# Performance work log

Measured on AMD Instinct MI355X. Metric: run time of the kernel, lower is better.

Reference implementation:

```python
import jax, jax.numpy as jnp
import numpy as np

N_NODES = 50000
N_EDGES = 800000
NUM_GRAPHS = 1024
IN_DIM = 25
DIM = 64
STEPS = 3


def setup_inputs() -> dict:
    key = jax.random.key(0)
    ks = jax.random.split(key, 16)
    s = 0.1
    return {
        "x": jax.random.normal(ks[0], (N_NODES, IN_DIM), dtype=jnp.float32),
        "edge_index": jax.random.randint(ks[1], (2, N_EDGES), 0, N_NODES),
        "batch": jnp.sort(jax.random.randint(ks[2], (N_NODES,), 0, NUM_GRAPHS)),
        "W0": jax.random.normal(ks[3], (IN_DIM, DIM), dtype=jnp.float32) * s,
        "b0": jnp.zeros((DIM,), jnp.float32),
        "Wc": jax.random.normal(ks[4], (DIM, DIM), dtype=jnp.float32) * s,
        "bc": jnp.zeros((DIM,), jnp.float32),
        "Wih": jax.random.normal(ks[5], (4 * DIM, 2 * DIM), dtype=jnp.float32) * s,
        "Whh": jax.random.normal(ks[6], (4 * DIM, DIM), dtype=jnp.float32) * s,
        "bih": jnp.zeros((4 * DIM,), jnp.float32),
        "bhh": jnp.zeros((4 * DIM,), jnp.float32),
        "W1": jax.random.normal(ks[7], (2 * DIM, DIM), dtype=jnp.float32) * s,
        "b1": jnp.zeros((DIM,), jnp.float32),
        "W2": jax.random.normal(ks[8], (DIM, 1), dtype=jnp.float32) * s,
        "b2": jnp.zeros((1,), jnp.float32),
    }


def _lstm_cell(xin, h, c, Wih, Whh, bih, bhh):
    gates = xin @ Wih.T + h @ Whh.T + bih + bhh  # [B, 4*DIM]
    i, f, g, o = jnp.split(gates, 4, axis=-1)
    i, f, o = jax.nn.sigmoid(i), jax.nn.sigmoid(f), jax.nn.sigmoid(o)
    g = jnp.tanh(g)
    c = f * c + i * g
    h = o * jnp.tanh(c)
    return h, c


def reference(x, edge_index, batch, W0, b0, Wc, bc, Wih, Whh, bih, bhh, W1, b1, W2, b2):
    n = x.shape[0]
    # lin0 + relu
    h = jax.nn.relu(x @ W0 + b0)
    # GCNConv: x @ W, add self loops, symmetric normalization, scatter-add
    hw = h @ Wc
    loops = jnp.arange(n, dtype=edge_index.dtype)
    row = jnp.concatenate([edge_index[0], loops])  # sources
    col = jnp.concatenate([edge_index[1], loops])  # targets
    deg = jax.ops.segment_sum(jnp.ones_like(row, dtype=hw.dtype), col, num_segments=n)
    dinv = jnp.where(deg > 0, jax.lax.rsqrt(deg), 0.0)
    norm = dinv[row] * dinv[col]
    msg = hw[row] * norm[:, None]  # [E+N, DIM] gather
    agg = jax.ops.segment_sum(msg, col, num_segments=n) + bc
    h = jax.nn.relu(agg)
    # Set2Set pooling with LSTM, 3 processing steps
    B = NUM_GRAPHS
    q_star = jnp.zeros((B, 2 * DIM), h.dtype)
    hs = jnp.zeros((B, DIM), h.dtype)
    cs = jnp.zeros((B, DIM), h.dtype)
    for _ in range(STEPS):
        hs, cs = _lstm_cell(q_star, hs, cs, Wih, Whh, bih, bhh)
        q = hs  # [B, DIM]
        e = jnp.sum(h * q[batch], axis=-1)  # [N]
        emax = jax.ops.segment_max(e, batch, num_segments=B)
        a = jnp.exp(e - emax[batch])
        asum = jax.ops.segment_sum(a, batch, num_segments=B)
        a = a / asum[batch]
        r = jax.ops.segment_sum(a[:, None] * h, batch, num_segments=B)  # [B, DIM]
        q_star = jnp.concatenate([q, r], axis=-1)
    out = jax.nn.relu(q_star @ W1 + b1)
    out = out @ W2 + b2
    return out.reshape(-1)
```

## Files before the change

### kernel.cpp

```cpp
#include <hip/hip_runtime.h>
#include <hip/hip_fp16.h>
#include <math.h>

#define N_NODES 50000
#define N_EDGES 800000
#define NGRAPH  1024
#define IN_DIM  25
#define DIM     64

#define NBK 98
#define CAP 12288
#define NPB 128
#define NFILL (NBK * 4)
#define NBIN 391
#define CROWS 128

__device__ inline float wsum(float v) {
#pragma unroll
  for (int off = 32; off > 0; off >>= 1) v += __shfl_xor(v, off, 64);
  return v;
}
__device__ inline int wsumi(int v) {
#pragma unroll
  for (int off = 32; off > 0; off >>= 1) v += __shfl_xor(v, off, 64);
  return v;
}
__device__ inline float sigmoidf(float x) { return 1.f / (1.f + expf(-x)); }

__global__ __launch_bounds__(256) void k_bin(const int* __restrict__ ei,
    int* __restrict__ gcur, int* __restrict__ pairs,
    const float* __restrict__ Wih, const float* __restrict__ Whh,
    float* __restrict__ WT) {
  __shared__ int hist[NBK];
  __shared__ int sbase[NBK];
  __shared__ int lbase[NBK];
  __shared__ int sorted[2048];
  int t = threadIdx.x;
  if (blockIdx.x == NBIN) {
    for (int i = t; i < 3 * DIM * 4 * DIM; i += 256) {
      int k = i >> 8, tt = i & 255;
      WT[i] = (k < 2 * DIM) ? Wih[tt * 2 * DIM + k] : Whh[tt * DIM + (k - 2 * DIM)];
    }
    return;
  }
  int base = blockIdx.x * 2048;
  for (int i = t; i < NBK; i += 256) hist[i] = 0;
  __syncthreads();
  int pk[8], bkt[8], rank[8];
#pragma unroll
  for (int k = 0; k < 8; k++) {
    int e = base + k * 256 + t;
    if (e < N_EDGES) {
      int row = ei[e];
      int col = ei[N_EDGES + e];
      int b = col >> 9;
      bkt[k] = b;
      rank[k] = atomicAdd(&hist[b], 1);
      pk[k] = (b << 25) | ((col & 511) << 16) | row;
    } else {
      bkt[k] = -1;
    }
  }
  __syncthreads();
  if (t < 64) {
    int i0 = 2 * t, i1 = 2 * t + 1;
    int v0 = (i0 < NBK) ? hist[i0] : 0;
    int v1 = (i1 < NBK) ? hist[i1] : 0;
    int loc = v0 + v1, x = loc;
#pragma unroll
    for (int d = 1; d < 64; d <<= 1) {
      int y = __shfl_up(x, d, 64);
      if (t >= d) x += y;
    }
    int excl = x - loc;
    if (i0 < NBK) sbase[i0] = excl;
    if (i1 < NBK) sbase[i1] = excl + v0;
  }
  __syncthreads();
#pragma unroll
  for (int k = 0; k < 8; k++)
    if (bkt[k] >= 0) sorted[sbase[bkt[k]] + rank[k]] = pk[k];
  for (int i = t; i < NBK; i += 256)
    lbase[i] = hist[i] ? atomicAdd(&gcur[i], hist[i]) : 0;
  __syncthreads();
  int ntot = min(2048, N_EDGES - base);
  for (int i = t; i < ntot; i += 256) {
    int p = sorted[i];
    int b = ((unsigned)p) >> 25;
    int gpos = lbase[b] + (i - sbase[b]);
    if (gpos < CAP) pairs[(size_t)b * CAP + gpos] = p & 0x1FFFFFF;
  }
}

__global__ __launch_bounds__(256) void k_fillcsr(const int* __restrict__ pairs,
    const int* __restrict__ gcur, int* __restrict__ cnt,
    float* __restrict__ dinv, int* __restrict__ adj) {
  __shared__ int hist[NPB];
  __shared__ int sbase, sbef;
  int b = blockIdx.x;
  int cb = b >> 2, sub = b & 3;
  int t = threadIdx.x, lane = t & 63;
  int lo = sub * NPB;
  int nb0 = cb * 512 + lo;
  if (t < NPB) hist[t] = 0;
  if (t == 0) { sbef = 0; sbase = 0; }
  __syncthreads();
  int ne = min(gcur[cb], CAP);
  const int* pp = pairs + (size_t)cb * CAP;
  const int4* pp4 = (const int4*)pp;
  int ne4 = ne >> 2;
  int mybef = 0;
  for (int i = t; i < ne4; i += 256) {
    int4 p4 = pp4[i];
    int c0 = p4.x >> 16, c1 = p4.y >> 16, c2 = p4.z >> 16, c3 = p4.w >> 16;
    if ((unsigned)(c0 - lo) < NPB) atomicAdd(&hist[c0 - lo], 1);
    if ((unsigned)(c1 - lo) < NPB) atomicAdd(&hist[c1 - lo], 1);
    if ((unsigned)(c2 - lo) < NPB) atomicAdd(&hist[c2 - lo], 1);
    if ((unsigned)(c3 - lo) < NPB) atomicAdd(&hist[c3 - lo], 1);
    mybef += (c0 < lo) + (c1 < lo) + (c2 < lo) + (c3 < lo);
  }
  for (int i = (ne4 << 2) + t; i < ne; i += 256) {
    int c = pp[i] >> 16;
    if ((unsigned)(c - lo) < NPB) atomicAdd(&hist[c - lo], 1);
    mybef += (c < lo);
  }
  mybef = wsumi(mybef);
  if (lane == 0 && mybef) atomicAdd(&sbef, mybef);
  __syncthreads();
  if (t < NPB) {
    int node = nb0 + t;
    if (node < N_NODES) dinv[node] = rsqrtf((float)(hist[t] + 1));
  }
  if (t < 64) {
    int v = 0;
    for (int i = t; i < cb; i += 64) v += gcur[i];
    v = wsumi(v);
    if (t == 0) sbase = v;
  }
  __syncthreads();
  int basev = sbase + sbef;
  if (t < 64) {
    int v0 = hist[2 * t], v1 = hist[2 * t + 1];
    int loc = v0 + v1;
    int x = loc;
#pragma unroll
    for (int d = 1; d < 64; d <<= 1) {
      int y = __shfl_up(x, d, 64);
      if (t >= d) x += y;
    }
    int excl = basev + x - loc;
    hist[2 * t] = excl;
    hist[2 * t + 1] = excl + v0;
  }
  __syncthreads();
  if (t < NPB) {
    int node = nb0 + t;
    if (node < N_NODES) cnt[node] = hist[t];
  }
  if (b == NFILL - 1 && t == 0) cnt[N_NODES] = N_EDGES;
  __syncthreads();
  for (int i = t; i < ne4; i += 256) {
    int4 p4 = pp4[i];
#pragma unroll
    for (int u = 0; u < 4; u++) {
      int p = (&p4.x)[u];
      unsigned cl = (unsigned)((p >> 16) - lo);
      if (cl < NPB) {
        int slot = atomicAdd(&hist[cl], 1);
        adj[slot] = p & 0xFFFF;
      }
    }
  }
  for (int i = (ne4 << 2) + t; i < ne; i += 256) {
    int p = pp[i];
    unsigned cl = (unsigned)((p >> 16) - lo);
    if (cl < NPB) {
      int slot = atomicAdd(&hist[cl], 1);
      adj[slot] = p & 0xFFFF;
    }
  }
}

__global__ __launch_bounds__(256) void k_lin0(const float* __restrict__ x,
    const float* __restrict__ W0, const float* __restrict__ b0,
    const float* __restrict__ Wc, const float* __restrict__ dinv,
    __half* __restrict__ hw16) {
  __shared__ float sx[64][IN_DIM + 1];
  __shared__ float sW0[IN_DIM][DIM];
  __shared__ float sh[64][DIM + 4];
  __shared__ float sWc[DIM][DIM];
  int t = threadIdx.x;
  int row0 = blockIdx.x * 64;
  for (int i = t; i < 64 * IN_DIM; i += 256) {
    int r = i / IN_DIM, k = i - r * IN_DIM;
    int row = row0 + r;
    sx[r][k] = (row < N_NODES) ? x[row * IN_DIM + k] : 0.f;
  }
  for (int i = t; i < IN_DIM * DIM; i += 256) sW0[i >> 6][i & 63] = W0[i];
  for (int i = t; i < DIM * DIM; i += 256) sWc[i >> 6][i & 63] = Wc[i];
  __syncthreads();
  int tc = (t & 15) * 4;
  int tr = (t >> 4) * 4;
  float acc[4][4];
  {
    float4 bb = *(const float4*)&b0[tc];
#pragma unroll
    for (int i = 0; i < 4; i++) {
      acc[i][0] = bb.x; acc[i][1] = bb.y; acc[i][2] = bb.z; acc[i][3] = bb.w;
    }
  }
#pragma unroll
  for (int k = 0; k < IN_DIM; k++) {
    float4 w = *(const float4*)&sW0[k][tc];
#pragma unroll
    for (int i = 0; i < 4; i++) {
      float a = sx[tr + i][k];
      acc[i][0] += a * w.x; acc[i][1] += a * w.y;
      acc[i][2] += a * w.z; acc[i][3] += a * w.w;
    }
  }
#pragma unroll
  for (int i = 0; i < 4; i++) {
    sh[tr + i][tc + 0] = fmaxf(acc[i][0], 0.f);
    sh[tr + i][tc + 1] = fmaxf(acc[i][1], 0.f);
    sh[tr + i][tc + 2] = fmaxf(acc[i][2], 0.f);
    sh[tr + i][tc + 3] = fmaxf(acc[i][3], 0.f);
  }
  __syncthreads();
#pragma unroll
  for (int i = 0; i < 4; i++) acc[i][0] = acc[i][1] = acc[i][2] = acc[i][3] = 0.f;
#pragma unroll 8
  for (int k = 0; k < DIM; k++) {
    float4 w = *(const float4*)&sWc[k][tc];
#pragma unroll
    for (int i = 0; i < 4; i++) {
      float a = sh[tr + i][k];
      acc[i][0] += a * w.x; acc[i][1] += a * w.y;
      acc[i][2] += a * w.z; acc[i][3] += a * w.w;
    }
  }
  float2* hwf2 = (float2*)hw16;
#pragma unroll
  for (int i = 0; i < 4; i++) {
    int row = row0 + tr + i;
    if (row < N_NODES) {
      float dv = dinv[row];
      float2 st;
      ((__half2*)&st)[0] = __floats2half2_rn(acc[i][0] * dv, acc[i][1] * dv);
      ((__half2*)&st)[1] = __floats2half2_rn(acc[i][2] * dv, acc[i][3] * dv);
      hwf2[(size_t)row * 16 + (t & 15)] = st;
    }
  }
}

__global__ __launch_bounds__(256) void k_gather(const int* __restrict__ adj,
    const int* __restrict__ cnt, const __half* __restrict__ hw16,
    const float* __restrict__ dinv, const float4* __restrict__ bc4,
    __half* __restrict__ h16) {
  int t = threadIdx.x;
  int lane = t & 63, wave = t >> 6;
  int q = lane >> 4, ql = lane & 15;
  int node = blockIdx.x * 16 + wave * 4 + q;
  if (node >= N_NODES) return;
  const float2* hwf2 = (const float2*)hw16;
  int s = cnt[node], eend = cnt[node + 1];
  float di = dinv[node];
  float4 a0 = make_float4(0.f, 0.f, 0.f, 0.f), a1 = a0, a2 = a0, a3 = a0;
  {
    float2 raw = hwf2[(size_t)node * 16 + ql];
    float2 f0 = __half22float2(((const __half2*)&raw)[0]);
    float2 f1 = __half22float2(((const __half2*)&raw)[1]);
    a0.x = f0.x; a0.y = f0.y; a0.z = f1.x; a0.w = f1.y;
  }
  int qb = q << 4;
  int idx = 0;
  if (s < eend && ql < eend - s) idx = adj[s + ql];
  for (int cb = s; cb < eend; cb += 16) {
    int cn = min(16, eend - cb);
    int nb = cb + 16;
    int nidx = 0;
    if (nb < eend && ql < eend - nb) nidx = adj[nb + ql];
    int j = 0;
    for (; j + 4 <= cn; j += 4) {
      int r0 = __shfl(idx, qb + j, 64), r1 = __shfl(idx, qb + j + 1, 64);
      int r2 = __shfl(idx, qb + j + 2, 64), r3 = __shfl(idx, qb + j + 3, 64);
      float2 w0 = hwf2[(size_t)r0 * 16 + ql];
      float2 w1 = hwf2[(size_t)r1 * 16 + ql];
      float2 w2 = hwf2[(size_t)r2 * 16 + ql];
      float2 w3 = hwf2[(size_t)r3 * 16 + ql];
      float2 f;
      f = __half22float2(((const __half2*)&w0)[0]); a0.x += f.x; a0.y += f.y;
      f = __half22float2(((const __half2*)&w0)[1]); a0.z += f.x; a0.w += f.y;
      f = __half22float2(((const __half2*)&w1)[0]); a1.x += f.x; a1.y += f.y;
      f = __half22float2(((const __half2*)&w1)[1]); a1.z += f.x; a1.w += f.y;
      f = __half22float2(((const __half2*)&w2)[0]); a2.x += f.x; a2.y += f.y;
      f = __half22float2(((const __half2*)&w2)[1]); a2.z += f.x; a2.w += f.y;
      f = __half22float2(((const __half2*)&w3)[0]); a3.x += f.x; a3.y += f.y;
      f = __half22float2(((const __half2*)&w3)[1]); a3.z += f.x; a3.w += f.y;
    }
    for (; j < cn; j++) {
      int r = __shfl(idx, qb + j, 64);
      float2 w = hwf2[(size_t)r * 16 + ql];
      float2 f;
      f = __half22float2(((const __half2*)&w)[0]); a0.x += f.x; a0.y += f.y;
      f = __half22float2(((const __half2*)&w)[1]); a0.z += f.x; a0.w += f.y;
    }
    idx = nidx;
  }
  float4 bb = bc4[ql];
  float ox = fmaxf(((a0.x + a1.x) + (a2.x + a3.x)) * di + bb.x, 0.f);
  float oy = fmaxf(((a0.y + a1.y) + (a2.y + a3.y)) * di + bb.y, 0.f);
  float oz = fmaxf(((a0.z + a1.z) + (a2.z + a3.z)) * di + bb.z, 0.f);
  float ow = fmaxf(((a0.w + a1.w) + (a2.w + a3.w)) * di + bb.w, 0.f);
  float2 st;
  ((__half2*)&st)[0] = __floats2half2_rn(ox, oy);
  ((__half2*)&st)[1] = __floats2half2_rn(oz, ow);
  ((float2*)h16)[(size_t)node * 16 + ql] = st;
}

__global__ __launch_bounds__(256) void k_set2set(
    const __half* __restrict__ h16, const int* __restrict__ batch,
    const float* __restrict__ WT, const float* __restrict__ bih,
    const float* __restrict__ bhh, const float* __restrict__ W1,
    const float* __restrict__ b1, const float* __restrict__ W2,
    const float* __restrict__ b2, float* __restrict__ out) {
  int b = blockIdx.x, t = threadIdx.x;
  int wave = t >> 6, lane = t & 63;
  int q = lane >> 4, ql = lane & 15;
  int qid = (wave << 2) + q;
  __shared__ float2 hcf2[CROWS * 16];
  __shared__ float qs[2 * DIM];
  __shared__ float hsl[DIM], csl[DIM];
  __shared__ float gates[4 * DIM];
  __shared__ float red[16 * DIM];
  __shared__ float lred[16], wmax[16];
  __shared__ int seg[2];
  const float2* h2 = (const float2*)h16;
  if (t < 2) {
    int g = b + t;
    int lo = 0, hi = N_NODES;
    if (g == NGRAPH) lo = N_NODES;
    else while (lo < hi) { int mid = (lo + hi) >> 1; if (batch[mid] < g) lo = mid + 1; else hi = mid; }
    seg[t] = lo;
  }
  if (t < 2 * DIM) qs[t] = 0.f;
  if (t < DIM) { hsl[t] = 0.f; csl[t] = 0.f; }
  __syncthreads();
  int s = seg[0], eend = seg[1];
  int nc = min(eend - s, CROWS);
  for (int i = t; i < nc * 16; i += 256)
    hcf2[i] = h2[(size_t)(s + (i >> 4)) * 16 + (i & 15)];
  __syncthreads();
  float bsum = bih[t] + bhh[t];
  for (int step = 0; step < 3; step++) {
    float g = bsum;
    if (step > 0) {
      const float* wp = WT + t;
      float g1 = 0.f;
#pragma unroll 8
      for (int k = 0; k < 2 * DIM; k += 2) {
        g += qs[k] * wp[k * 4 * DIM];
        g1 += qs[k + 1] * wp[(k + 1) * 4 * DIM];
      }
#pragma unroll 8
      for (int k = 0; k < DIM; k += 2) {
        g += hsl[k] * wp[(2 * DIM + k) * 4 * DIM];
        g1 += hsl[k + 1] * wp[(2 * DIM + k + 1) * 4 * DIM];
      }
      g += g1;
    }
    gates[t] = g;
    __syncthreads();
    if (t < DIM) {
      float ig = sigmoidf(gates[t]);
      float fg = sigmoidf(gates[DIM + t]);
      float gg = tanhf(gates[2 * DIM + t]);
      float og = sigmoidf(gates[3 * DIM + t]);
      float c = fg * csl[t] + ig * gg;
      csl[t] = c;
      float hh = og * tanhf(c);
      hsl[t] = hh;
      qs[t] = hh;
    }
    __syncthreads();
    float4 qf = *(const float4*)&hsl[4 * ql];
    float m_w = -INFINITY, l_w = 0.f;
    float4 racc = make_float4(0.f, 0.f, 0.f, 0.f);
    for (int j = s + qid; j < eend; j += 16) {
      int lj = j - s;
      float2 raw = (lj < CROWS) ? hcf2[lj * 16 + ql]
                                : h2[(size_t)j * 16 + ql];
      float2 f0 = __half22float2(((const __half2*)&raw)[0]);
      float2 f1 = __half22float2(((const __half2*)&raw)[1]);
      float p = f0.x * qf.x + f0.y * qf.y + f1.x * qf.z + f1.y * qf.w;
#pragma unroll
      for (int off = 1; off < 16; off <<= 1) p += __shfl_xor(p, off, 64);
      float m_new = fmaxf(m_w, p);
      float scale = __expf(m_w - m_new);
      float a = __expf(p - m_new);
      racc.x = racc.x * scale + a * f0.x;
      racc.y = racc.y * scale + a * f0.y;
      racc.z = racc.z * scale + a * f1.x;
      racc.w = racc.w * scale + a * f1.y;
      l_w = l_w * scale + a;
      m_w = m_new;
    }
    *(float4*)&red[qid * DIM + 4 * ql] = racc;
    if (ql == 0) { lred[qid] = l_w; wmax[qid] = m_w; }
    __syncthreads();
    if (t < DIM) {
      float m_b = -1e30f;
      for (int i = 0; i < 16; i++) m_b = fmaxf(m_b, wmax[i]);
      float r = 0.f, l = 0.f;
      for (int i = 0; i < 16; i++) {
        float e = __expf(wmax[i] - m_b);
        r += red[i * DIM + t] * e;
        l += lred[i] * e;
      }
      qs[DIM + t] = (l > 0.f) ? r / l : 0.f;
    }
    __syncthreads();
  }
  if (t < DIM) {
    float acc = b1[t];
#pragma unroll
    for (int k = 0; k < 2 * DIM; k++) acc += qs[k] * W1[k * DIM + t];
    acc = fmaxf(acc, 0.f);
    float v = wsum(acc * W2[t]);
    if (t == 0) out[b] = v + b2[0];
  }
}

extern "C" void kernel_launch(void* const* d_in, const int* in_sizes, int n_in,
                              void* d_out, int out_size, void* d_ws, size_t ws_size,
                              hipStream_t stream) {
  const float* x    = (const float*)d_in[0];
  const int*   ei   = (const int*)d_in[1];
  const int*   batch= (const int*)d_in[2];
  const float* W0   = (const float*)d_in[3];
  const float* b0   = (const float*)d_in[4];
  const float* Wc   = (const float*)d_in[5];
  const float* bc   = (const float*)d_in[6];
  const float* Wih  = (const float*)d_in[7];
  const float* Whh  = (const float*)d_in[8];
  const float* bih  = (const float*)d_in[9];
  const float* bhh  = (const float*)d_in[10];
  const float* W1   = (const float*)d_in[11];
  const float* b1   = (const float*)d_in[12];
  const float* W2   = (const float*)d_in[13];
  const float* b2   = (const float*)d_in[14];
  float* out = (float*)d_out;

  __half* hw16 = (__half*)d_ws;
  __half* h16  = hw16 + (size_t)N_NODES * DIM;
  float* dinv  = (float*)(h16 + (size_t)N_NODES * DIM);
  float* WT    = dinv + N_NODES;
  int* cnt     = (int*)(WT + 3 * DIM * 4 * DIM);
  int* adj     = cnt + N_NODES + 4;
  int* gcur    = adj + N_EDGES;
  int* pairs   = gcur + NBK + 2;

  hipMemsetAsync(gcur, 0, NBK * sizeof(int), stream);
  k_bin<<<NBIN + 1, 256, 0, stream>>>(ei, gcur, pairs, Wih, Whh, WT);
  k_fillcsr<<<NFILL, 256, 0, stream>>>(pairs, gcur, cnt, dinv, adj);
  k_lin0<<<(N_NODES + 63) / 64, 256, 0, stream>>>(x, W0, b0, Wc, dinv, hw16);
  k_gather<<<(N_NODES + 15) / 16, 256, 0, stream>>>(adj, cnt, hw16, dinv,
                                                    (const float4*)bc, h16);
  k_set2set<<<NGRAPH, 256, 0, stream>>>(h16, batch, WT, bih, bhh, W1, b1, W2, b2, out);
}
```

Measured before the change: 198.9 us.

## Replace CSR build with 64-node buckets and shared-memory atomic aggregation

Edges are now binned into 782 buckets of 64 target nodes, which matches the k_lin0 block size. The separate CSR fill kernel is removed. k_lin0 computes the degree histogram and dinv for its bucket, and a new k_agg kernel scatters gathered half-precision rows into a shared-memory accumulator with LDS float atomics instead of walking per-node adjacency lists. This drops one kernel launch and the adj/cnt writes, at the cost of heavy LDS atomic contention, fewer blocks, and nondeterministic summation order. CAP 1536 per bucket relies on the uniform random degree distribution and silently drops overflow edges.

```diff
diff --git a/kernel.cpp b/kernel.cpp
--- a/kernel.cpp
+++ b/kernel.cpp
@@ -8,19 +8,12 @@
 #define IN_DIM  25
 #define DIM     64
 
-#define NBK 98
-#define CAP 12288
-#define NPB 128
-#define NFILL (NBK * 4)
+#define NBKB 782
+#define CAP  1536
 #define NBIN 391
 #define CROWS 128
 
 __device__ inline float wsum(float v) {
-#pragma unroll
-  for (int off = 32; off > 0; off >>= 1) v += __shfl_xor(v, off, 64);
-  return v;
-}
-__device__ inline int wsumi(int v) {
 #pragma unroll
   for (int off = 32; off > 0; off >>= 1) v += __shfl_xor(v, off, 64);
   return v;
@@ -31,9 +24,9 @@
     int* __restrict__ gcur, int* __restrict__ pairs,
     const float* __restrict__ Wih, const float* __restrict__ Whh,
     float* __restrict__ WT) {
-  __shared__ int hist[NBK];
-  __shared__ int sbase[NBK];
-  __shared__ int lbase[NBK];
+  __shared__ int hist[NBKB];
+  __shared__ int sbase[NBKB];
+  __shared__ int lbase[NBKB];
   __shared__ int sorted[2048];
   int t = threadIdx.x;
   if (blockIdx.x == NBIN) {
@@ -44,7 +37,7 @@
     return;
   }
   int base = blockIdx.x * 2048;
-  for (int i = t; i < NBK; i += 256) hist[i] = 0;
+  for (int i = t; i < NBKB; i += 256) hist[i] = 0;
   __syncthreads();
   int pk[8], bkt[8], rank[8];
 #pragma unroll
@@ -53,144 +46,68 @@
     if (e < N_EDGES) {
       int row = ei[e];
       int col = ei[N_EDGES + e];
-      int b = col >> 9;
+      int b = col >> 6;
       bkt[k] = b;
       rank[k] = atomicAdd(&hist[b], 1);
-      pk[k] = (b << 25) | ((col & 511) << 16) | row;
+      pk[k] = (int)(((unsigned)b << 22) | ((unsigned)(col & 63) << 16) | (unsigned)row);
     } else {
       bkt[k] = -1;
     }
   }
   __syncthreads();
   if (t < 64) {
-    int i0 = 2 * t, i1 = 2 * t + 1;
-    int v0 = (i0 < NBK) ? hist[i0] : 0;
-    int v1 = (i1 < NBK) ? hist[i1] : 0;
-    int loc = v0 + v1, x = loc;
+    int v[13];
+    int loc = 0;
+#pragma unroll
+    for (int i = 0; i < 13; i++) {
+      int idx = t * 13 + i;
+      v[i] = (idx < NBKB) ? hist[idx] : 0;
+      loc += v[i];
+    }
+    int x = loc;
 #pragma unroll
     for (int d = 1; d < 64; d <<= 1) {
       int y = __shfl_up(x, d, 64);
       if (t >= d) x += y;
     }
     int excl = x - loc;
-    if (i0 < NBK) sbase[i0] = excl;
-    if (i1 < NBK) sbase[i1] = excl + v0;
+#pragma unroll
+    for (int i = 0; i < 13; i++) {
+      int idx = t * 13 + i;
+      if (idx < NBKB) sbase[idx] = excl;
+      excl += v[i];
+    }
   }
   __syncthreads();
 #pragma unroll
   for (int k = 0; k < 8; k++)
     if (bkt[k] >= 0) sorted[sbase[bkt[k]] + rank[k]] = pk[k];
-  for (int i = t; i < NBK; i += 256)
+  for (int i = t; i < NBKB; i += 256)
     lbase[i] = hist[i] ? atomicAdd(&gcur[i], hist[i]) : 0;
   __syncthreads();
   int ntot = min(2048, N_EDGES - base);
   for (int i = t; i < ntot; i += 256) {
     int p = sorted[i];
-    int b = ((unsigned)p) >> 25;
+    int b = ((unsigned)p) >> 22;
     int gpos = lbase[b] + (i - sbase[b]);
-    if (gpos < CAP) pairs[(size_t)b * CAP + gpos] = p & 0x1FFFFFF;
-  }
-}
-
-__global__ __launch_bounds__(256) void k_fillcsr(const int* __restrict__ pairs,
-    const int* __restrict__ gcur, int* __restrict__ cnt,
-    float* __restrict__ dinv, int* __restrict__ adj) {
-  __shared__ int hist[NPB];
-  __shared__ int sbase, sbef;
-  int b = blockIdx.x;
-  int cb = b >> 2, sub = b & 3;
-  int t = threadIdx.x, lane = t & 63;
-  int lo = sub * NPB;
-  int nb0 = cb * 512 + lo;
-  if (t < NPB) hist[t] = 0;
-  if (t == 0) { sbef = 0; sbase = 0; }
-  __syncthreads();
-  int ne = min(gcur[cb], CAP);
-  const int* pp = pairs + (size_t)cb * CAP;
-  const int4* pp4 = (const int4*)pp;
-  int ne4 = ne >> 2;
-  int mybef = 0;
-  for (int i = t; i < ne4; i += 256) {
-    int4 p4 = pp4[i];
-    int c0 = p4.x >> 16, c1 = p4.y >> 16, c2 = p4.z >> 16, c3 = p4.w >> 16;
-    if ((unsigned)(c0 - lo) < NPB) atomicAdd(&hist[c0 - lo], 1);
-    if ((unsigned)(c1 - lo) < NPB) atomicAdd(&hist[c1 - lo], 1);
-    if ((unsigned)(c2 - lo) < NPB) atomicAdd(&hist[c2 - lo], 1);
-    if ((unsigned)(c3 - lo) < NPB) atomicAdd(&hist[c3 - lo], 1);
-    mybef += (c0 < lo) + (c1 < lo) + (c2 < lo) + (c3 < lo);
-  }
-  for (int i = (ne4 << 2) + t; i < ne; i += 256) {
-    int c = pp[i] >> 16;
-    if ((unsigned)(c - lo) < NPB) atomicAdd(&hist[c - lo], 1);
-    mybef += (c < lo);
-  }
-  mybef = wsumi(mybef);
-  if (lane == 0 && mybef) atomicAdd(&sbef, mybef);
-  __syncthreads();
-  if (t < NPB) {
-    int node = nb0 + t;
-    if (node < N_NODES) dinv[node] = rsqrtf((float)(hist[t] + 1));
-  }
-  if (t < 64) {
-    int v = 0;
-    for (int i = t; i < cb; i += 64) v += gcur[i];
-    v = wsumi(v);
-    if (t == 0) sbase = v;
-  }
-  __syncthreads();
-  int basev = sbase + sbef;
-  if (t < 64) {
-    int v0 = hist[2 * t], v1 = hist[2 * t + 1];
-    int loc = v0 + v1;
-    int x = loc;
-#pragma unroll
-    for (int d = 1; d < 64; d <<= 1) {
-      int y = __shfl_up(x, d, 64);
-      if (t >= d) x += y;
-    }
-    int excl = basev + x - loc;
-    hist[2 * t] = excl;
-    hist[2 * t + 1] = excl + v0;
-  }
-  __syncthreads();
-  if (t < NPB) {
-    int node = nb0 + t;
-    if (node < N_NODES) cnt[node] = hist[t];
-  }
-  if (b == NFILL - 1 && t == 0) cnt[N_NODES] = N_EDGES;
-  __syncthreads();
-  for (int i = t; i < ne4; i += 256) {
-    int4 p4 = pp4[i];
-#pragma unroll
-    for (int u = 0; u < 4; u++) {
-      int p = (&p4.x)[u];
-      unsigned cl = (unsigned)((p >> 16) - lo);
-      if (cl < NPB) {
-        int slot = atomicAdd(&hist[cl], 1);
-        adj[slot] = p & 0xFFFF;
-      }
-    }
-  }
-  for (int i = (ne4 << 2) + t; i < ne; i += 256) {
-    int p = pp[i];
-    unsigned cl = (unsigned)((p >> 16) - lo);
-    if (cl < NPB) {
-      int slot = atomicAdd(&hist[cl], 1);
-      adj[slot] = p & 0xFFFF;
-    }
+    if (gpos < CAP) pairs[(size_t)b * CAP + gpos] = p & 0x3FFFFF;
   }
 }
 
 __global__ __launch_bounds__(256) void k_lin0(const float* __restrict__ x,
     const float* __restrict__ W0, const float* __restrict__ b0,
-    const float* __restrict__ Wc, const float* __restrict__ dinv,
+    const float* __restrict__ Wc, const int* __restrict__ pairs,
+    const int* __restrict__ gcur, float* __restrict__ dinv,
     __half* __restrict__ hw16) {
   __shared__ float sx[64][IN_DIM + 1];
   __shared__ float sW0[IN_DIM][DIM];
   __shared__ float sh[64][DIM + 4];
   __shared__ float sWc[DIM][DIM];
+  __shared__ int histd[64];
   int t = threadIdx.x;
   int row0 = blockIdx.x * 64;
+  if (t < 64) histd[t] = 0;
+  __syncthreads();
   for (int i = t; i < 64 * IN_DIM; i += 256) {
     int r = i / IN_DIM, k = i - r * IN_DIM;
     int row = row0 + r;
@@ -198,6 +115,21 @@
   }
   for (int i = t; i < IN_DIM * DIM; i += 256) sW0[i >> 6][i & 63] = W0[i];
   for (int i = t; i < DIM * DIM; i += 256) sWc[i >> 6][i & 63] = Wc[i];
+  {
+    int ne = min(gcur[blockIdx.x], CAP);
+    const int* pp = pairs + (size_t)blockIdx.x * CAP;
+    const int4* pp4 = (const int4*)pp;
+    int ne4 = ne >> 2;
+    for (int i = t; i < ne4; i += 256) {
+      int4 p4 = pp4[i];
+      atomicAdd(&histd[(p4.x >> 16) & 63], 1);
+      atomicAdd(&histd[(p4.y >> 16) & 63], 1);
+      atomicAdd(&histd[(p4.z >> 16) & 63], 1);
+      atomicAdd(&histd[(p4.w >> 16) & 63], 1);
+    }
+    for (int i = (ne4 << 2) + t; i < ne; i += 256)
+      atomicAdd(&histd[(pp[i] >> 16) & 63], 1);
+  }
   __syncthreads();
   int tc = (t & 15) * 4;
   int tr = (t >> 4) * 4;
@@ -239,12 +171,16 @@
       acc[i][2] += a * w.z; acc[i][3] += a * w.w;
     }
   }
+  if (t < 64) {
+    int node = row0 + t;
+    if (node < N_NODES) dinv[node] = rsqrtf((float)(histd[t] + 1));
+  }
   float2* hwf2 = (float2*)hw16;
 #pragma unroll
   for (int i = 0; i < 4; i++) {
     int row = row0 + tr + i;
     if (row < N_NODES) {
-      float dv = dinv[row];
+      float dv = rsqrtf((float)(histd[tr + i] + 1));
       float2 st;
       ((__half2*)&st)[0] = __floats2half2_rn(acc[i][0] * dv, acc[i][1] * dv);
       ((__half2*)&st)[1] = __floats2half2_rn(acc[i][2] * dv, acc[i][3] * dv);
@@ -253,69 +189,56 @@
   }
 }
 
-__global__ __launch_bounds__(256) void k_gather(const int* __restrict__ adj,
-    const int* __restrict__ cnt, const __half* __restrict__ hw16,
+__global__ __launch_bounds__(256) void k_agg(const int* __restrict__ pairs,
+    const int* __restrict__ gcur, const __half* __restrict__ hw16,
     const float* __restrict__ dinv, const float4* __restrict__ bc4,
     __half* __restrict__ h16) {
-  int t = threadIdx.x;
-  int lane = t & 63, wave = t >> 6;
-  int q = lane >> 4, ql = lane & 15;
-  int node = blockIdx.x * 16 + wave * 4 + q;
-  if (node >= N_NODES) return;
+  __shared__ float acc[64][69];
+  int b = blockIdx.x, t = threadIdx.x;
+  int lane = t & 63, wave = t >> 6, q = lane >> 4, ql = lane & 15;
+  for (int i = t; i < 64 * 69; i += 256) ((float*)acc)[i] = 0.f;
+  __syncthreads();
+  int ne = min(gcur[b], CAP);
+  const int* pp = pairs + (size_t)b * CAP;
   const float2* hwf2 = (const float2*)hw16;
-  int s = cnt[node], eend = cnt[node + 1];
-  float di = dinv[node];
-  float4 a0 = make_float4(0.f, 0.f, 0.f, 0.f), a1 = a0, a2 = a0, a3 = a0;
-  {
+  for (int base = wave * 64; base < ne; base += 256) {
+    int p = (base + lane < ne) ? pp[base + lane] : -1;
+#pragma unroll
+    for (int j = 0; j < 64; j += 4) {
+      int pe = __shfl(p, j + q, 64);
+      if (pe >= 0) {
+        int row = pe & 0xFFFF;
+        int cl = (pe >> 16) & 63;
+        float2 raw = hwf2[(size_t)row * 16 + ql];
+        float2 f0 = __half22float2(((const __half2*)&raw)[0]);
+        float2 f1 = __half22float2(((const __half2*)&raw)[1]);
+        float* ap = &acc[cl][4 * ql];
+        atomicAdd(ap + 0, f0.x);
+        atomicAdd(ap + 1, f0.y);
+        atomicAdd(ap + 2, f1.x);
+        atomicAdd(ap + 3, f1.y);
+      }
+    }
+  }
+  __syncthreads();
+  int qid = (wave << 2) + q;
+  for (int nl = qid; nl < 64; nl += 16) {
+    int node = b * 64 + nl;
+    if (node >= N_NODES) continue;
     float2 raw = hwf2[(size_t)node * 16 + ql];
     float2 f0 = __half22float2(((const __half2*)&raw)[0]);
     float2 f1 = __half22float2(((const __half2*)&raw)[1]);
-    a0.x = f0.x; a0.y = f0.y; a0.z = f1.x; a0.w = f1.y;
-  }
-  int qb = q << 4;
-  int idx = 0;
-  if (s < eend && ql < eend - s) idx = adj[s + ql];
-  for (int cb = s; cb < eend; cb += 16) {
-    int cn = min(16, eend - cb);
-    int nb = cb + 16;
-    int nidx = 0;
-    if (nb < eend && ql < eend - nb) nidx = adj[nb + ql];
-    int j = 0;
-    for (; j + 4 <= cn; j += 4) {
-      int r0 = __shfl(idx, qb + j, 64), r1 = __shfl(idx, qb + j + 1, 64);
-      int r2 = __shfl(idx, qb + j + 2, 64), r3 = __shfl(idx, qb + j + 3, 64);
-      float2 w0 = hwf2[(size_t)r0 * 16 + ql];
-      float2 w1 = hwf2[(size_t)r1 * 16 + ql];
-      float2 w2 = hwf2[(size_t)r2 * 16 + ql];
-      float2 w3 = hwf2[(size_t)r3 * 16 + ql];
-      float2 f;
-      f = __half22float2(((const __half2*)&w0)[0]); a0.x += f.x; a0.y += f.y;
-      f = __half22float2(((const __half2*)&w0)[1]); a0.z += f.x; a0.w += f.y;
-      f = __half22float2(((const __half2*)&w1)[0]); a1.x += f.x; a1.y += f.y;
-      f = __half22float2(((const __half2*)&w1)[1]); a1.z += f.x; a1.w += f.y;
-      f = __half22float2(((const __half2*)&w2)[0]); a2.x += f.x; a2.y += f.y;
-      f = __half22float2(((const __half2*)&w2)[1]); a2.z += f.x; a2.w += f.y;
-      f = __half22float2(((const __half2*)&w3)[0]); a3.x += f.x; a3.y += f.y;
-      f = __half22float2(((const __half2*)&w3)[1]); a3.z += f.x; a3.w += f.y;
-    }
-    for (; j < cn; j++) {
-      int r = __shfl(idx, qb + j, 64);
-      float2 w = hwf2[(size_t)r * 16 + ql];
-      float2 f;
-      f = __half22float2(((const __half2*)&w)[0]); a0.x += f.x; a0.y += f.y;
-      f = __half22float2(((const __half2*)&w)[1]); a0.z += f.x; a0.w += f.y;
-    }
-    idx = nidx;
-  }
-  float4 bb = bc4[ql];
-  float ox = fmaxf(((a0.x + a1.x) + (a2.x + a3.x)) * di + bb.x, 0.f);
-  float oy = fmaxf(((a0.y + a1.y) + (a2.y + a3.y)) * di + bb.y, 0.f);
-  float oz = fmaxf(((a0.z + a1.z) + (a2.z + a3.z)) * di + bb.z, 0.f);
-  float ow = fmaxf(((a0.w + a1.w) + (a2.w + a3.w)) * di + bb.w, 0.f);
-  float2 st;
-  ((__half2*)&st)[0] = __floats2half2_rn(ox, oy);
-  ((__half2*)&st)[1] = __floats2half2_rn(oz, ow);
-  ((float2*)h16)[(size_t)node * 16 + ql] = st;
+    float di = dinv[node];
+    float4 bb = bc4[ql];
+    float ox = fmaxf((acc[nl][4 * ql + 0] + f0.x) * di + bb.x, 0.f);
+    float oy = fmaxf((acc[nl][4 * ql + 1] + f0.y) * di + bb.y, 0.f);
+    float oz = fmaxf((acc[nl][4 * ql + 2] + f1.x) * di + bb.z, 0.f);
+    float ow = fmaxf((acc[nl][4 * ql + 3] + f1.y) * di + bb.w, 0.f);
+    float2 st;
+    ((__half2*)&st)[0] = __floats2half2_rn(ox, oy);
+    ((__half2*)&st)[1] = __floats2half2_rn(oz, ow);
+    ((float2*)h16)[(size_t)node * 16 + ql] = st;
+  }
 }
 
 __global__ __launch_bounds__(256) void k_set2set(
@@ -455,16 +378,12 @@
   __half* h16  = hw16 + (size_t)N_NODES * DIM;
   float* dinv  = (float*)(h16 + (size_t)N_NODES * DIM);
   float* WT    = dinv + N_NODES;
-  int* cnt     = (int*)(WT + 3 * DIM * 4 * DIM);
-  int* adj     = cnt + N_NODES + 4;
-  int* gcur    = adj + N_EDGES;
-  int* pairs   = gcur + NBK + 2;
-
-  hipMemsetAsync(gcur, 0, NBK * sizeof(int), stream);
+  int* gcur    = (int*)(WT + 3 * DIM * 4 * DIM);
+  int* pairs   = gcur + NBKB + 2;
+
+  hipMemsetAsync(gcur, 0, NBKB * sizeof(int), stream);
   k_bin<<<NBIN + 1, 256, 0, stream>>>(ei, gcur, pairs, Wih, Whh, WT);
-  k_fillcsr<<<NFILL, 256, 0, stream>>>(pairs, gcur, cnt, dinv, adj);
-  k_lin0<<<(N_NODES + 63) / 64, 256, 0, stream>>>(x, W0, b0, Wc, dinv, hw16);
-  k_gather<<<(N_NODES + 15) / 16, 256, 0, stream>>>(adj, cnt, hw16, dinv,
-                                                    (const float4*)bc, h16);
+  k_lin0<<<NBKB, 256, 0, stream>>>(x, W0, b0, Wc, pairs, gcur, dinv, hw16);
+  k_agg<<<NBKB, 256, 0, stream>>>(pairs, gcur, hw16, dinv, (const float4*)bc, h16);
   k_set2set<<<NGRAPH, 256, 0, stream>>>(h16, batch, WT, bih, bhh, W1, b1, W2, b2, out);
 }
```

Result: slower. 513.8 us (+158.3%).
